# Kernel tuning notes

Measured on AMD Instinct MI355X. Metric: run time of the kernel, lower is better.

Reference implementation:

```python
import jax, jax.numpy as jnp
import numpy as np

N = 50000      # nodes
E = 400000     # directed edges
F_IN = 128     # input features
H0, C0 = 4, 64     # layer0: 4 heads x 64, concat -> 256
H1, C1 = 1, 256    # layer1: 1 head x 256, mean/concat -> 256
NCLS = 10
SLOPE = 0.2    # PyG GATConv leaky_relu negative_slope


def setup_inputs() -> dict:
    key = jax.random.key(0)
    ks = jax.random.split(key, 20)
    g = lambda k, shape, fan_in: jax.random.normal(k, shape, jnp.float32) * (1.0 / np.sqrt(fan_in))
    x = jax.random.normal(ks[0], (N, F_IN), jnp.float32)
    edge_index = jax.random.randint(ks[1], (2, E), 0, N)
    return {
        "x": x,
        "edge_index": edge_index,
        # GATConv layer 0: 128 -> 4 heads x 64, concat
        "W0": g(ks[2], (F_IN, H0 * C0), F_IN),
        "a_src0": g(ks[3], (H0, C0), C0),
        "a_dst0": g(ks[4], (H0, C0), C0),
        "b0": jnp.zeros((H0 * C0,), jnp.float32),
        # GATConv layer 1: 256 -> 1 head x 256, averaged
        "W1": g(ks[5], (H0 * C0, H1 * C1), H0 * C0),
        "a_src1": g(ks[6], (H1, C1), C1),
        "a_dst1": g(ks[7], (H1, C1), C1),
        "b1": jnp.zeros((C1,), jnp.float32),
        # MLP head 256 -> 512 -> 1024 -> NCLS
        "lw1": g(ks[8], (256, 512), 256), "lb1": jnp.zeros((512,), jnp.float32),
        "lw2": g(ks[9], (512, 1024), 512), "lb2": jnp.zeros((1024,), jnp.float32),
        "lw3": g(ks[10], (1024, NCLS), 1024), "lb3": jnp.zeros((NCLS,), jnp.float32),
    }


def _gat_conv(x, src, dst, valid, W, a_src, a_dst, b, heads, ch, concat):
    """PyG GATConv (eval mode, dropout=0): gather -> edge attention ->
    softmax over incoming edges per target -> scatter-sum aggregate."""
    n = x.shape[0]
    h = (x @ W).reshape(n, heads, ch)                      # [N,H,C]
    alpha_src = jnp.sum(h * a_src[None], axis=-1)          # [N,H]
    alpha_dst = jnp.sum(h * a_dst[None], axis=-1)          # [N,H]
    e = jax.nn.leaky_relu(alpha_src[src] + alpha_dst[dst], SLOPE)  # [Etot,H]
    e = jnp.where(valid[:, None], e, -1e9)                 # removed self-loops
    emax = jax.lax.stop_gradient(jax.ops.segment_max(e, dst, num_segments=n))
    w = jnp.exp(e - emax[dst]) * valid[:, None].astype(e.dtype)
    denom = jax.ops.segment_sum(w, dst, num_segments=n)    # [N,H] (>0: self-loops)
    w = w / denom[dst]
    out = jax.ops.segment_sum(h[src] * w[..., None], dst, num_segments=n)  # [N,H,C]
    out = out.reshape(n, heads * ch) if concat else out.mean(axis=1)
    return out + b


def reference(x, edge_index, W0, a_src0, a_dst0, b0, W1, a_src1, a_dst1, b1,
              lw1, lb1, lw2, lb2, lw3, lb3):
    n = x.shape[0]
    s0, d0 = edge_index[0], edge_index[1]
    loop = jnp.arange(n, dtype=s0.dtype)
    src = jnp.concatenate([s0, loop])
    dst = jnp.concatenate([d0, loop])
    valid = jnp.concatenate([s0 != d0, jnp.ones((n,), bool)])  # remove+add self-loops
    h = jax.nn.relu(_gat_conv(x, src, dst, valid, W0, a_src0, a_dst0, b0, H0, C0, True))
    h = jax.nn.relu(_gat_conv(h, src, dst, valid, W1, a_src1, a_dst1, b1, H1, C1, False))
    h = jax.nn.relu(h @ lw1 + lb1)
    h = jax.nn.relu(h @ lw2 + lb2)
    h = jax.nn.relu(h @ lw3 + lb3)
    return jax.nn.softmax(h, axis=1)
```

## Files before the change

kernel.cpp:

```cpp
#include <hip/hip_runtime.h>
#include <cstdint>
#include <cstddef>

#define F_IN   128
#define SLOPE  0.2f

typedef unsigned short u16;
typedef __attribute__((ext_vector_type(8))) short     bf16x8;
typedef __attribute__((ext_vector_type(8))) unsigned short u16x8;
typedef __attribute__((ext_vector_type(4))) unsigned short u16x4;
typedef __attribute__((ext_vector_type(4))) float     f32x4;

__device__ __forceinline__ u16 f2bf(float f) {
    unsigned u = __float_as_uint(f);
    unsigned r = u + 0x7FFFu + ((u >> 16) & 1u);
    return (u16)(r >> 16);
}
__device__ __forceinline__ float bf2f(u16 h) {
    return __uint_as_float(((unsigned)h) << 16);
}

__device__ __forceinline__ float lrelu(float v) { return v >= 0.f ? v : SLOPE * v; }

__global__ void alphas0_k(const u16* __restrict__ h0, const float* __restrict__ a_src,
                          const float* __restrict__ a_dst, float* __restrict__ asrc,
                          float* __restrict__ adst, int N) {
    int gid = blockIdx.x * blockDim.x + threadIdx.x;
    int n = gid >> 6, lane = gid & 63;
    if (n >= N) return;
    int h = lane >> 4, c0 = lane << 2;
    u16x4 hv = *(const u16x4*)(h0 + (size_t)n * 256 + c0);
    float4 ws = *(const float4*)(a_src + c0);
    float4 wd = *(const float4*)(a_dst + c0);
    float s1 = bf2f(hv[0]) * ws.x + bf2f(hv[1]) * ws.y + bf2f(hv[2]) * ws.z + bf2f(hv[3]) * ws.w;
    float s2 = bf2f(hv[0]) * wd.x + bf2f(hv[1]) * wd.y + bf2f(hv[2]) * wd.z + bf2f(hv[3]) * wd.w;
    #pragma unroll
    for (int off = 8; off; off >>= 1) {
        s1 += __shfl_xor(s1, off);
        s2 += __shfl_xor(s2, off);
    }
    if ((lane & 15) == 0) { asrc[n * 4 + h] = s1; adst[n * 4 + h] = s2; }
}

__global__ void alphas1_k(const u16* __restrict__ h1, const float* __restrict__ a_src,
                          const float* __restrict__ a_dst, float* __restrict__ asrc,
                          float* __restrict__ adst, int N) {
    int gid = blockIdx.x * blockDim.x + threadIdx.x;
    int n = gid >> 6, lane = gid & 63;
    if (n >= N) return;
    int c0 = lane << 2;
    u16x4 hv = *(const u16x4*)(h1 + (size_t)n * 256 + c0);
    float4 ws = *(const float4*)(a_src + c0);
    float4 wd = *(const float4*)(a_dst + c0);
    float s1 = bf2f(hv[0]) * ws.x + bf2f(hv[1]) * ws.y + bf2f(hv[2]) * ws.z + bf2f(hv[3]) * ws.w;
    float s2 = bf2f(hv[0]) * wd.x + bf2f(hv[1]) * wd.y + bf2f(hv[2]) * wd.z + bf2f(hv[3]) * wd.w;
    #pragma unroll
    for (int off = 32; off; off >>= 1) {
        s1 += __shfl_xor(s1, off);
        s2 += __shfl_xor(s2, off);
    }
    if (lane == 0) { asrc[n] = s1; adst[n] = s2; }
}

__global__ void deg_init(int* __restrict__ deg, int N) {
    int i = blockIdx.x * blockDim.x + threadIdx.x;
    if (i < N) deg[i] = 1;
}

__global__ void count_deg(const int* __restrict__ ei, int* __restrict__ deg, int E) {
    int e = blockIdx.x * blockDim.x + threadIdx.x;
    if (e >= E) return;
    int s = ei[e], d = ei[E + e];
    if (s != d) atomicAdd(&deg[d], 1);
}

__global__ void scan1(const int* __restrict__ deg, int* __restrict__ part,
                      int* __restrict__ bsum, int N) {
    __shared__ int sm[256];
    int i = blockIdx.x * 256 + threadIdx.x;
    int v = (i < N) ? deg[i] : 0;
    sm[threadIdx.x] = v; __syncthreads();
    for (int off = 1; off < 256; off <<= 1) {
        int tv = (threadIdx.x >= off) ? sm[threadIdx.x - off] : 0;
        __syncthreads();
        sm[threadIdx.x] += tv;
        __syncthreads();
    }
    if (i < N) part[i] = sm[threadIdx.x] - v;
    if (threadIdx.x == 255) bsum[blockIdx.x] = sm[255];
}

__global__ void scan2(int* __restrict__ bsum, int nb) {
    __shared__ int sm[256];
    __shared__ int carry;
    if (threadIdx.x == 0) carry = 0;
    __syncthreads();
    for (int base = 0; base < nb; base += 256) {
        int i = base + threadIdx.x;
        int v = (i < nb) ? bsum[i] : 0;
        sm[threadIdx.x] = v; __syncthreads();
        for (int off = 1; off < 256; off <<= 1) {
            int tv = (threadIdx.x >= off) ? sm[threadIdx.x - off] : 0;
            __syncthreads();
            sm[threadIdx.x] += tv;
            __syncthreads();
        }
        if (i < nb) bsum[i] = sm[threadIdx.x] - v + carry;
        __syncthreads();
        if (threadIdx.x == 0) carry += sm[255];
        __syncthreads();
    }
}

__global__ void scan3(const int* __restrict__ deg, const int* __restrict__ part,
                      const int* __restrict__ bsum, int* __restrict__ rowp,
                      int* __restrict__ cursor, int N) {
    int i = blockIdx.x * blockDim.x + threadIdx.x;
    if (i >= N) return;
    int r = part[i] + bsum[i >> 8];
    rowp[i] = r;
    cursor[i] = r;
    if (i == N - 1) rowp[N] = r + deg[i];
}

__global__ void scatter_k(const int* __restrict__ ei, int* __restrict__ cursor,
                          int* __restrict__ csr, int E, int N) {
    int e = blockIdx.x * blockDim.x + threadIdx.x;
    if (e >= E + N) return;
    int s, d;
    if (e < E) { s = ei[e]; d = ei[E + e]; if (s == d) return; }
    else       { s = d = e - E; }
    int pos = atomicAdd(&cursor[d], 1);
    csr[pos] = s;
}

__global__ void gat_gather0(const int* __restrict__ csr, const int* __restrict__ rowp,
                            const u16* __restrict__ h0, const float* __restrict__ asrc,
                            const float* __restrict__ adst, const float* __restrict__ b,
                            float* __restrict__ outx, int N) {
    int gid = blockIdx.x * blockDim.x + threadIdx.x;
    int n = gid >> 6, lane = gid & 63;
    if (n >= N) return;
    int h = lane >> 4, c0 = lane << 2;
    int beg = rowp[n], end = rowp[n + 1];
    float4 ad = *(const float4*)(adst + (size_t)n * 4);
    float m0 = -1e30f, m1 = -1e30f, m2 = -1e30f, m3 = -1e30f;
    for (int i = beg + lane; i < end; i += 64) {
        int s = csr[i];
        float4 as = *(const float4*)(asrc + (size_t)s * 4);
        m0 = fmaxf(m0, lrelu(as.x + ad.x));
        m1 = fmaxf(m1, lrelu(as.y + ad.y));
        m2 = fmaxf(m2, lrelu(as.z + ad.z));
        m3 = fmaxf(m3, lrelu(as.w + ad.w));
    }
    #pragma unroll
    for (int off = 32; off; off >>= 1) {
        m0 = fmaxf(m0, __shfl_xor(m0, off));
        m1 = fmaxf(m1, __shfl_xor(m1, off));
        m2 = fmaxf(m2, __shfl_xor(m2, off));
        m3 = fmaxf(m3, __shfl_xor(m3, off));
    }
    float mh  = (h == 0) ? m0   : (h == 1) ? m1   : (h == 2) ? m2   : m3;
    float adh = (h == 0) ? ad.x : (h == 1) ? ad.y : (h == 2) ? ad.z : ad.w;
    float acc0 = 0.f, acc1 = 0.f, acc2 = 0.f, acc3 = 0.f, den = 0.f;
    #pragma unroll 2
    for (int i = beg; i < end; ++i) {
        int s = csr[i];
        float w = __expf(lrelu(asrc[(size_t)s * 4 + h] + adh) - mh);
        den += w;
        u16x4 hv = *(const u16x4*)(h0 + (size_t)s * 256 + c0);
        acc0 += w * bf2f(hv[0]);
        acc1 += w * bf2f(hv[1]);
        acc2 += w * bf2f(hv[2]);
        acc3 += w * bf2f(hv[3]);
    }
    float inv = 1.f / den;
    float4 bb = *(const float4*)(b + c0);
    float4 ov;
    ov.x = acc0 * inv + bb.x; ov.x = ov.x > 0.f ? ov.x : 0.f;
    ov.y = acc1 * inv + bb.y; ov.y = ov.y > 0.f ? ov.y : 0.f;
    ov.z = acc2 * inv + bb.z; ov.z = ov.z > 0.f ? ov.z : 0.f;
    ov.w = acc3 * inv + bb.w; ov.w = ov.w > 0.f ? ov.w : 0.f;
    *(float4*)(outx + (size_t)n * 256 + c0) = ov;
}

__global__ void gat_gather1(const int* __restrict__ csr, const int* __restrict__ rowp,
                            const u16* __restrict__ h1, const float* __restrict__ asrc,
                            const float* __restrict__ adst, const float* __restrict__ b,
                            u16* __restrict__ outx, int N) {
    int gid = blockIdx.x * blockDim.x + threadIdx.x;
    int n = gid >> 6, lane = gid & 63;
    if (n >= N) return;
    int c0 = lane << 2;
    int beg = rowp[n], end = rowp[n + 1];
    float adn = adst[n];
    float mx = -1e30f;
    for (int i = beg + lane; i < end; i += 64) {
        int s = csr[i];
        mx = fmaxf(mx, lrelu(asrc[s] + adn));
    }
    #pragma unroll
    for (int off = 32; off; off >>= 1) mx = fmaxf(mx, __shfl_xor(mx, off));
    float acc0 = 0.f, acc1 = 0.f, acc2 = 0.f, acc3 = 0.f, den = 0.f;
    #pragma unroll 2
    for (int i = beg; i < end; ++i) {
        int s = csr[i];
        float w = __expf(lrelu(asrc[s] + adn) - mx);
        den += w;
        u16x4 hv = *(const u16x4*)(h1 + (size_t)s * 256 + c0);
        acc0 += w * bf2f(hv[0]);
        acc1 += w * bf2f(hv[1]);
        acc2 += w * bf2f(hv[2]);
        acc3 += w * bf2f(hv[3]);
    }
    float inv = 1.f / den;
    float4 bb = *(const float4*)(b + c0);
    float v0 = acc0 * inv + bb.x, v1 = acc1 * inv + bb.y;
    float v2 = acc2 * inv + bb.z, v3 = acc3 * inv + bb.w;
    u16x4 ov;
    ov[0] = f2bf(v0 > 0.f ? v0 : 0.f);
    ov[1] = f2bf(v1 > 0.f ? v1 : 0.f);
    ov[2] = f2bf(v2 > 0.f ? v2 : 0.f);
    ov[3] = f2bf(v3 > 0.f ? v3 : 0.f);
    *(u16x4*)(outx + (size_t)n * 256 + c0) = ov;
}

__global__ void pack_w(const float* __restrict__ W, u16* __restrict__ out,
                       int K, int Nsrc, int NT) {
    int gid  = blockIdx.x * blockDim.x + threadIdx.x;
    int lane = gid & 63, frag = gid >> 6;
    int KT = K >> 5;
    if (frag >= KT * NT) return;
    int nt = frag % NT, kt = frag / NT;
    int n  = nt * 16 + (lane & 15);
    int k0 = kt * 32 + ((lane >> 4) << 3);
    u16x8 v8;
    #pragma unroll
    for (int i = 0; i < 8; ++i) {
        float v = (n < Nsrc) ? W[(size_t)(k0 + i) * Nsrc + n] : 0.f;
        v8[i] = f2bf(v);
    }
    *(u16x8*)(out + (size_t)(frag * 64 + lane) * 8) = v8;
}

__global__ void pack_w_hl(const float* __restrict__ W, u16* __restrict__ ohi,
                          u16* __restrict__ olo, int K, int Nsrc, int NT) {
    int gid  = blockIdx.x * blockDim.x + threadIdx.x;
    int lane = gid & 63, frag = gid >> 6;
    int KT = K >> 5;
    if (frag >= KT * NT) return;
    int nt = frag % NT, kt = frag / NT;
    int n  = nt * 16 + (lane & 15);
    int k0 = kt * 32 + ((lane >> 4) << 3);
    u16x8 h8, l8;
    #pragma unroll
    for (int i = 0; i < 8; ++i) {
        float v = (n < Nsrc) ? W[(size_t)(k0 + i) * Nsrc + n] : 0.f;
        u16 hi = f2bf(v);
        h8[i] = hi;
        l8[i] = f2bf(v - bf2f(hi));
    }
    *(u16x8*)(ohi + (size_t)(frag * 64 + lane) * 8) = h8;
    *(u16x8*)(olo + (size_t)(frag * 64 + lane) * 8) = l8;
}

__device__ __forceinline__ bf16x8 lds_afrag(const u16* buf, int Kdim, int row0, int kt, int lane) {
    int row = row0 + (lane & 15);
    int k   = kt * 32 + ((lane >> 4) << 3);
    int idx = (row * Kdim + k) ^ ((row & 7) << 3);
    return *(const bf16x8*)(buf + idx);
}

__global__ __launch_bounds__(512) void gemm_mfma(
    const float* __restrict__ A, const u16* __restrict__ bhi, const u16* __restrict__ blo,
    u16* __restrict__ C, int M, int K) {
    __shared__ __align__(16) u16 Ahi[64 * 256];
    __shared__ __align__(16) u16 Alo[64 * 256];
    int t = threadIdx.x, lane = t & 63, w = t >> 6;
    int row0 = blockIdx.x * 64;
    int K4 = K >> 2;

    for (int idx = t; idx < 64 * K4; idx += 512) {
        int row = idx / K4, kq = (idx % K4) << 2;
        int gr = row0 + row;
        float4 v = make_float4(0.f, 0.f, 0.f, 0.f);
        if (gr < M) v = *(const float4*)(A + (size_t)gr * K + kq);
        u16x4 h4, l4;
        float vv[4] = {v.x, v.y, v.z, v.w};
        #pragma unroll
        for (int i = 0; i < 4; ++i) {
            u16 hi = f2bf(vv[i]);
            h4[i] = hi;
            l4[i] = f2bf(vv[i] - bf2f(hi));
        }
        int sidx = (row * K + kq) ^ ((row & 7) << 3);
        *(u16x4*)(Ahi + sidx) = h4;
        *(u16x4*)(Alo + sidx) = l4;
    }
    __syncthreads();

    int KT = K >> 5;
    f32x4 acc[4][2] = {};
    for (int kt = 0; kt < KT; ++kt) {
        bf16x8 ah[4], al[4];
        #pragma unroll
        for (int mt = 0; mt < 4; ++mt) {
            ah[mt] = lds_afrag(Ahi, K, mt * 16, kt, lane);
            al[mt] = lds_afrag(Alo, K, mt * 16, kt, lane);
        }
        #pragma unroll
        for (int nt = 0; nt < 2; ++nt) {
            int ntg = w * 2 + nt;
            size_t fo = ((size_t)(kt * 16 + ntg) * 64 + lane) * 8;
            bf16x8 bh = *(const bf16x8*)(bhi + fo);
            bf16x8 bl = *(const bf16x8*)(blo + fo);
            #pragma unroll
            for (int mt = 0; mt < 4; ++mt) {
                acc[mt][nt] = __builtin_amdgcn_mfma_f32_16x16x32_bf16(al[mt], bh, acc[mt][nt], 0, 0, 0);
                acc[mt][nt] = __builtin_amdgcn_mfma_f32_16x16x32_bf16(ah[mt], bl, acc[mt][nt], 0, 0, 0);
                acc[mt][nt] = __builtin_amdgcn_mfma_f32_16x16x32_bf16(ah[mt], bh, acc[mt][nt], 0, 0, 0);
            }
        }
    }

    #pragma unroll
    for (int mt = 0; mt < 4; ++mt)
        #pragma unroll
        for (int nt = 0; nt < 2; ++nt) {
            int col = w * 32 + nt * 16 + (lane & 15);
            #pragma unroll
            for (int j = 0; j < 4; ++j) {
                int gr = row0 + mt * 16 + ((lane >> 4) << 2) + j;
                if (gr < M) C[(size_t)gr * 256 + col] = f2bf(acc[mt][nt][j]);
            }
        }
}

#define NB 32

__global__ __launch_bounds__(512) void mlp_mfma(
    const u16* __restrict__ m0,
    const u16* __restrict__ w1p, const float* __restrict__ lb1,
    const u16* __restrict__ w2p, const float* __restrict__ lb2,
    const u16* __restrict__ w3p, const float* __restrict__ lb3,
    float* __restrict__ out, int N) {
    __shared__ __align__(16) u16 ldsA0[32 * 256];
    __shared__ __align__(16) u16 ldsA1[32 * 512];
    __shared__ __align__(16) u16 ldsA2[32 * 1024];
    __shared__ float slog[32 * 16];

    int t = threadIdx.x, lane = t & 63, w = t >> 6;
    int nb = blockIdx.x * NB;

    slog[t] = 0.f;

    bf16x8 b1A[4], b1B[4];
    #pragma unroll
    for (int nt = 0; nt < 4; ++nt)
        b1A[nt] = *(const bf16x8*)(w1p + ((size_t)(w * 4 + nt) * 64 + lane) * 8);

    #pragma unroll
    for (int u = 0; u < 2; ++u) {
        int unit = t + u * 512;
        int row = unit >> 5, kb = (unit & 31) << 3;
        int gn = nb + row;
        u16x8 v8;
        if (gn < N) v8 = *(const u16x8*)(m0 + (size_t)gn * 256 + kb);
        else        v8 = (u16x8)0;
        int idx = (row * 256 + kb) ^ ((row & 7) << 3);
        *(u16x8*)(ldsA0 + idx) = v8;
    }
    __syncthreads();

    f32x4 acc1[2][4] = {};
    for (int kt = 0; kt < 8; kt += 2) {
        #pragma unroll
        for (int nt = 0; nt < 4; ++nt)
            b1B[nt] = *(const bf16x8*)(w1p + ((size_t)((kt + 1) * 32 + w * 4 + nt) * 64 + lane) * 8);
        {
            bf16x8 a0 = lds_afrag(ldsA0, 256, 0,  kt, lane);
            bf16x8 a1 = lds_afrag(ldsA0, 256, 16, kt, lane);
            #pragma unroll
            for (int nt = 0; nt < 4; ++nt) {
                acc1[0][nt] = __builtin_amdgcn_mfma_f32_16x16x32_bf16(a0, b1A[nt], acc1[0][nt], 0, 0, 0);
                acc1[1][nt] = __builtin_amdgcn_mfma_f32_16x16x32_bf16(a1, b1A[nt], acc1[1][nt], 0, 0, 0);
            }
        }
        if (kt + 2 < 8) {
            #pragma unroll
            for (int nt = 0; nt < 4; ++nt)
                b1A[nt] = *(const bf16x8*)(w1p + ((size_t)((kt + 2) * 32 + w * 4 + nt) * 64 + lane) * 8);
        }
        {
            bf16x8 a0 = lds_afrag(ldsA0, 256, 0,  kt + 1, lane);
            bf16x8 a1 = lds_afrag(ldsA0, 256, 16, kt + 1, lane);
            #pragma unroll
            for (int nt = 0; nt < 4; ++nt) {
                acc1[0][nt] = __builtin_amdgcn_mfma_f32_16x16x32_bf16(a0, b1B[nt], acc1[0][nt], 0, 0, 0);
                acc1[1][nt] = __builtin_amdgcn_mfma_f32_16x16x32_bf16(a1, b1B[nt], acc1[1][nt], 0, 0, 0);
            }
        }
    }

    bf16x8 b2A[8], b2B[8];
    #pragma unroll
    for (int nt = 0; nt < 8; ++nt)
        b2A[nt] = *(const bf16x8*)(w2p + ((size_t)(w * 8 + nt) * 64 + lane) * 8);

    #pragma unroll
    for (int mt = 0; mt < 2; ++mt)
        #pragma unroll
        for (int nt = 0; nt < 4; ++nt) {
            int col = w * 64 + nt * 16 + (lane & 15);
            float bv = lb1[col];
            #pragma unroll
            for (int j = 0; j < 4; ++j) {
                int row = mt * 16 + ((lane >> 4) << 2) + j;
                float v = acc1[mt][nt][j] + bv;
                v = v > 0.f ? v : 0.f;
                ldsA1[(row * 512 + col) ^ ((row & 7) << 3)] = f2bf(v);
            }
        }
    __syncthreads();

    f32x4 acc2[2][8] = {};
    for (int kt = 0; kt < 16; kt += 2) {
        #pragma unroll
        for (int nt = 0; nt < 8; ++nt)
            b2B[nt] = *(const bf16x8*)(w2p + ((size_t)((kt + 1) * 64 + w * 8 + nt) * 64 + lane) * 8);
        {
            bf16x8 a0 = lds_afrag(ldsA1, 512, 0,  kt, lane);
            bf16x8 a1 = lds_afrag(ldsA1, 512, 16, kt, lane);
            #pragma unroll
            for (int nt = 0; nt < 8; ++nt) {
                acc2[0][nt] = __builtin_amdgcn_mfma_f32_16x16x32_bf16(a0, b2A[nt], acc2[0][nt], 0, 0, 0);
                acc2[1][nt] = __builtin_amdgcn_mfma_f32_16x16x32_bf16(a1, b2A[nt], acc2[1][nt], 0, 0, 0);
            }
        }
        if (kt + 2 < 16) {
            #pragma unroll
            for (int nt = 0; nt < 8; ++nt)
                b2A[nt] = *(const bf16x8*)(w2p + ((size_t)((kt + 2) * 64 + w * 8 + nt) * 64 + lane) * 8);
        }
        {
            bf16x8 a0 = lds_afrag(ldsA1, 512, 0,  kt + 1, lane);
            bf16x8 a1 = lds_afrag(ldsA1, 512, 16, kt + 1, lane);
            #pragma unroll
            for (int nt = 0; nt < 8; ++nt) {
                acc2[0][nt] = __builtin_amdgcn_mfma_f32_16x16x32_bf16(a0, b2B[nt], acc2[0][nt], 0, 0, 0);
                acc2[1][nt] = __builtin_amdgcn_mfma_f32_16x16x32_bf16(a1, b2B[nt], acc2[1][nt], 0, 0, 0);
            }
        }
    }

    bf16x8 b3[4];
    #pragma unroll
    for (int kk = 0; kk < 4; ++kk)
        b3[kk] = *(const bf16x8*)(w3p + ((size_t)(w * 4 + kk) * 64 + lane) * 8);

    #pragma unroll
    for (int mt = 0; mt < 2; ++mt)
        #pragma unroll
        for (int nt = 0; nt < 8; ++nt) {
            int col = w * 128 + nt * 16 + (lane & 15);
            float bv = lb2[col];
            #pragma unroll
            for (int j = 0; j < 4; ++j) {
                int row = mt * 16 + ((lane >> 4) << 2) + j;
                float v = acc2[mt][nt][j] + bv;
                v = v > 0.f ? v : 0.f;
                ldsA2[(row * 1024 + col) ^ ((row & 7) << 3)] = f2bf(v);
            }
        }
    __syncthreads();

    {
        f32x4 acc[2] = {};
        #pragma unroll
        for (int kk = 0; kk < 4; ++kk) {
            int kt = w * 4 + kk;
            bf16x8 a0 = lds_afrag(ldsA2, 1024, 0,  kt, lane);
            bf16x8 a1 = lds_afrag(ldsA2, 1024, 16, kt, lane);
            acc[0] = __builtin_amdgcn_mfma_f32_16x16x32_bf16(a0, b3[kk], acc[0], 0, 0, 0);
            acc[1] = __builtin_amdgcn_mfma_f32_16x16x32_bf16(a1, b3[kk], acc[1], 0, 0, 0);
        }
        int col = lane & 15;
        #pragma unroll
        for (int mt = 0; mt < 2; ++mt)
            #pragma unroll
            for (int j = 0; j < 4; ++j) {
                int row = mt * 16 + ((lane >> 4) << 2) + j;
                atomicAdd(&slog[row * 16 + col], acc[mt][j]);
            }
    }
    __syncthreads();

    if (t < 32) {
        int gn = nb + t;
        if (gn < N) {
            float lg[10], m = -1e30f;
            #pragma unroll
            for (int k = 0; k < 10; ++k) {
                float v = slog[t * 16 + k] + lb3[k];
                v = v > 0.f ? v : 0.f;
                lg[k] = v;
                if (v > m) m = v;
            }
            float ssum = 0.f;
            #pragma unroll
            for (int k = 0; k < 10; ++k) { lg[k] = __expf(lg[k] - m); ssum += lg[k]; }
            float inv = 1.f / ssum;
            #pragma unroll
            for (int k = 0; k < 10; ++k) out[(size_t)gn * 10 + k] = lg[k] * inv;
        }
    }
}

extern "C" void kernel_launch(void* const* d_in, const int* in_sizes, int n_in,
                              void* d_out, int out_size, void* d_ws, size_t ws_size,
                              hipStream_t stream) {
    const float* x       = (const float*)d_in[0];
    const int*   ei      = (const int*)  d_in[1];
    const float* W0      = (const float*)d_in[2];
    const float* a_src0  = (const float*)d_in[3];
    const float* a_dst0  = (const float*)d_in[4];
    const float* b0      = (const float*)d_in[5];
    const float* W1      = (const float*)d_in[6];
    const float* a_src1  = (const float*)d_in[7];
    const float* a_dst1  = (const float*)d_in[8];
    const float* b1      = (const float*)d_in[9];
    const float* lw1     = (const float*)d_in[10];
    const float* lb1     = (const float*)d_in[11];
    const float* lw2     = (const float*)d_in[12];
    const float* lb2     = (const float*)d_in[13];
    const float* lw3     = (const float*)d_in[14];
    const float* lb3     = (const float*)d_in[15];
    float*       out     = (float*)d_out;

    const int N  = in_sizes[0] / F_IN;
    const int E  = in_sizes[1] / 2;
    const int ET = E + N;

    char* base = (char*)d_ws;
    size_t szHb = (size_t)N * 256 * sizeof(u16);
    u16*   hbf  = (u16*)base;
    float* bufG = (float*)(base + szHb);
    u16*   m0b  = (u16*)(base + szHb + (size_t)N * 256 * sizeof(float));
    float* asrc = (float*)(base + 2 * szHb + (size_t)N * 256 * sizeof(float));
    float* adst = asrc + (size_t)N * 4;
    u16*   w1p  = (u16*)(adst + (size_t)N * 4);
    u16*   w2p  = w1p + 256 * 512;
    u16*   w3p  = w2p + 512 * 1024;
    u16*   w0h  = w3p + 1024 * 16;
    u16*   w0l  = w0h + 128 * 256;
    u16*   w1h  = w0l + 128 * 256;
    u16*   w1l  = w1h + 256 * 256;
    int*   deg  = (int*)(w1l + 256 * 256);
    int*   rowp   = deg + N;
    int*   cursor = rowp + N + 1;
    int*   part   = cursor + N;
    int*   bsum   = part + N;
    int*   csr    = bsum + 256;

    const int TB  = 256;
    const int nb1 = (N + 255) / 256;
    const int gemm_grid = (N + 63) / 64;

    pack_w<<<(8  * 32 * 64 + TB - 1) / TB, TB, 0, stream>>>(lw1, w1p, 256,  512,  32);
    pack_w<<<(16 * 64 * 64 + TB - 1) / TB, TB, 0, stream>>>(lw2, w2p, 512,  1024, 64);
    pack_w<<<(32 * 1  * 64 + TB - 1) / TB, TB, 0, stream>>>(lw3, w3p, 1024, 10,   1);
    pack_w_hl<<<(4 * 16 * 64 + TB - 1) / TB, TB, 0, stream>>>(W0, w0h, w0l, 128, 256, 16);
    pack_w_hl<<<(8 * 16 * 64 + TB - 1) / TB, TB, 0, stream>>>(W1, w1h, w1l, 256, 256, 16);

    deg_init<<<nb1, TB, 0, stream>>>(deg, N);
    count_deg<<<(E + TB - 1) / TB, TB, 0, stream>>>(ei, deg, E);
    scan1<<<nb1, TB, 0, stream>>>(deg, part, bsum, N);
    scan2<<<1, TB, 0, stream>>>(bsum, nb1);
    scan3<<<nb1, TB, 0, stream>>>(deg, part, bsum, rowp, cursor, N);
    scatter_k<<<(ET + TB - 1) / TB, TB, 0, stream>>>(ei, cursor, csr, E, N);

    gemm_mfma<<<gemm_grid, 512, 0, stream>>>(x, w0h, w0l, hbf, N, 128);
    alphas0_k<<<(N * 64 + TB - 1) / TB, TB, 0, stream>>>(hbf, a_src0, a_dst0, asrc, adst, N);
    gat_gather0<<<((size_t)N * 64 + TB - 1) / TB, TB, 0, stream>>>(csr, rowp, hbf, asrc, adst, b0, bufG, N);

    gemm_mfma<<<gemm_grid, 512, 0, stream>>>(bufG, w1h, w1l, hbf, N, 256);
    alphas1_k<<<(N * 64 + TB - 1) / TB, TB, 0, stream>>>(hbf, a_src1, a_dst1, asrc, adst, N);
    gat_gather1<<<((size_t)N * 64 + TB - 1) / TB, TB, 0, stream>>>(csr, rowp, hbf, asrc, adst, b1, m0b, N);

    mlp_mfma<<<(N + NB - 1) / NB, 512, 0, stream>>>(m0b, w1p, lb1, w2p, lb2, w3p, lb3, out, N);
}
```

Before: 372.8 us.

## Split fused MLP into 64-row MFMA layers 1-2 kernel and separate layer-3 softmax kernel

Replaces the fully fused 32-row MLP kernel with a 64-row kernel computing layers 1 and 2 (writing the 1024-wide activation to global memory in bf16) plus a per-node wavefront kernel for the final 10-class layer and softmax. Work is processed in two halves so the intermediate fits in the reused workspace buffer. The larger row tile raises weight reuse per MFMA and removes LDS atomics, at the cost of extra global round-trip traffic for the intermediate and loss of the previous weight-load double buffering.

```diff
diff --git a/kernel.cpp b/kernel.cpp
--- a/kernel.cpp
+++ b/kernel.cpp
@@ -336,183 +336,136 @@
         }
 }
 
-#define NB 32
-
-__global__ __launch_bounds__(512) void mlp_mfma(
+__global__ __launch_bounds__(512) void mlp12(
     const u16* __restrict__ m0,
     const u16* __restrict__ w1p, const float* __restrict__ lb1,
     const u16* __restrict__ w2p, const float* __restrict__ lb2,
-    const u16* __restrict__ w3p, const float* __restrict__ lb3,
-    float* __restrict__ out, int N) {
-    __shared__ __align__(16) u16 ldsA0[32 * 256];
-    __shared__ __align__(16) u16 ldsA1[32 * 512];
-    __shared__ __align__(16) u16 ldsA2[32 * 1024];
-    __shared__ float slog[32 * 16];
+    u16* __restrict__ h2, int nbase, int M) {
+    __shared__ __align__(16) u16 ldsIn[64 * 256];
+    __shared__ __align__(16) u16 ldsA1[64 * 512];
 
     int t = threadIdx.x, lane = t & 63, w = t >> 6;
-    int nb = blockIdx.x * NB;
-
-    slog[t] = 0.f;
-
-    bf16x8 b1A[4], b1B[4];
-    #pragma unroll
-    for (int nt = 0; nt < 4; ++nt)
-        b1A[nt] = *(const bf16x8*)(w1p + ((size_t)(w * 4 + nt) * 64 + lane) * 8);
-
-    #pragma unroll
-    for (int u = 0; u < 2; ++u) {
+    int rb = blockIdx.x * 64;
+
+    #pragma unroll
+    for (int u = 0; u < 4; ++u) {
         int unit = t + u * 512;
         int row = unit >> 5, kb = (unit & 31) << 3;
-        int gn = nb + row;
+        int r = rb + row;
         u16x8 v8;
-        if (gn < N) v8 = *(const u16x8*)(m0 + (size_t)gn * 256 + kb);
-        else        v8 = (u16x8)0;
+        if (r < M) v8 = *(const u16x8*)(m0 + (size_t)(nbase + r) * 256 + kb);
+        else       v8 = (u16x8)0;
         int idx = (row * 256 + kb) ^ ((row & 7) << 3);
-        *(u16x8*)(ldsA0 + idx) = v8;
+        *(u16x8*)(ldsIn + idx) = v8;
     }
     __syncthreads();
 
-    f32x4 acc1[2][4] = {};
-    for (int kt = 0; kt < 8; kt += 2) {
-        #pragma unroll
-        for (int nt = 0; nt < 4; ++nt)
-            b1B[nt] = *(const bf16x8*)(w1p + ((size_t)((kt + 1) * 32 + w * 4 + nt) * 64 + lane) * 8);
-        {
-            bf16x8 a0 = lds_afrag(ldsA0, 256, 0,  kt, lane);
-            bf16x8 a1 = lds_afrag(ldsA0, 256, 16, kt, lane);
+    {
+        f32x4 acc1[4][4] = {};
+        for (int kt = 0; kt < 8; ++kt) {
+            bf16x8 a[4];
+            #pragma unroll
+            for (int mt = 0; mt < 4; ++mt) a[mt] = lds_afrag(ldsIn, 256, mt * 16, kt, lane);
             #pragma unroll
             for (int nt = 0; nt < 4; ++nt) {
-                acc1[0][nt] = __builtin_amdgcn_mfma_f32_16x16x32_bf16(a0, b1A[nt], acc1[0][nt], 0, 0, 0);
-                acc1[1][nt] = __builtin_amdgcn_mfma_f32_16x16x32_bf16(a1, b1A[nt], acc1[1][nt], 0, 0, 0);
+                bf16x8 b = *(const bf16x8*)(w1p + ((size_t)(kt * 32 + w * 4 + nt) * 64 + lane) * 8);
+                #pragma unroll
+                for (int mt = 0; mt < 4; ++mt)
+                    acc1[mt][nt] = __builtin_amdgcn_mfma_f32_16x16x32_bf16(a[mt], b, acc1[mt][nt], 0, 0, 0);
             }
         }
-        if (kt + 2 < 8) {
-            #pragma unroll
-            for (int nt = 0; nt < 4; ++nt)
-                b1A[nt] = *(const bf16x8*)(w1p + ((size_t)((kt + 2) * 32 + w * 4 + nt) * 64 + lane) * 8);
-        }
-        {
-            bf16x8 a0 = lds_afrag(ldsA0, 256, 0,  kt + 1, lane);
-            bf16x8 a1 = lds_afrag(ldsA0, 256, 16, kt + 1, lane);
+        #pragma unroll
+        for (int mt = 0; mt < 4; ++mt)
             #pragma unroll
             for (int nt = 0; nt < 4; ++nt) {
-                acc1[0][nt] = __builtin_amdgcn_mfma_f32_16x16x32_bf16(a0, b1B[nt], acc1[0][nt], 0, 0, 0);
-                acc1[1][nt] = __builtin_amdgcn_mfma_f32_16x16x32_bf16(a1, b1B[nt], acc1[1][nt], 0, 0, 0);
+                int col = w * 64 + nt * 16 + (lane & 15);
+                float bv = lb1[col];
+                #pragma unroll
+                for (int j = 0; j < 4; ++j) {
+                    int row = mt * 16 + ((lane >> 4) << 2) + j;
+                    float v = acc1[mt][nt][j] + bv;
+                    v = v > 0.f ? v : 0.f;
+                    ldsA1[(row * 512 + col) ^ ((row & 7) << 3)] = f2bf(v);
+                }
             }
-        }
-    }
-
-    bf16x8 b2A[8], b2B[8];
-    #pragma unroll
-    for (int nt = 0; nt < 8; ++nt)
-        b2A[nt] = *(const bf16x8*)(w2p + ((size_t)(w * 8 + nt) * 64 + lane) * 8);
-
-    #pragma unroll
-    for (int mt = 0; mt < 2; ++mt)
-        #pragma unroll
-        for (int nt = 0; nt < 4; ++nt) {
-            int col = w * 64 + nt * 16 + (lane & 15);
-            float bv = lb1[col];
-            #pragma unroll
-            for (int j = 0; j < 4; ++j) {
-                int row = mt * 16 + ((lane >> 4) << 2) + j;
-                float v = acc1[mt][nt][j] + bv;
-                v = v > 0.f ? v : 0.f;
-                ldsA1[(row * 512 + col) ^ ((row & 7) << 3)] = f2bf(v);
+    }
+    __syncthreads();
+
+    for (int ch = 0; ch < 2; ++ch) {
+        f32x4 acc[4][4] = {};
+        for (int kt = 0; kt < 16; ++kt) {
+            bf16x8 a[4];
+            #pragma unroll
+            for (int mt = 0; mt < 4; ++mt) a[mt] = lds_afrag(ldsA1, 512, mt * 16, kt, lane);
+            #pragma unroll
+            for (int nt = 0; nt < 4; ++nt) {
+                int ntg = ch * 32 + w * 4 + nt;
+                bf16x8 b = *(const bf16x8*)(w2p + ((size_t)(kt * 64 + ntg) * 64 + lane) * 8);
+                #pragma unroll
+                for (int mt = 0; mt < 4; ++mt)
+                    acc[mt][nt] = __builtin_amdgcn_mfma_f32_16x16x32_bf16(a[mt], b, acc[mt][nt], 0, 0, 0);
             }
         }
-    __syncthreads();
-
-    f32x4 acc2[2][8] = {};
-    for (int kt = 0; kt < 16; kt += 2) {
-        #pragma unroll
-        for (int nt = 0; nt < 8; ++nt)
-            b2B[nt] = *(const bf16x8*)(w2p + ((size_t)((kt + 1) * 64 + w * 8 + nt) * 64 + lane) * 8);
-        {
-            bf16x8 a0 = lds_afrag(ldsA1, 512, 0,  kt, lane);
-            bf16x8 a1 = lds_afrag(ldsA1, 512, 16, kt, lane);
-            #pragma unroll
-            for (int nt = 0; nt < 8; ++nt) {
-                acc2[0][nt] = __builtin_amdgcn_mfma_f32_16x16x32_bf16(a0, b2A[nt], acc2[0][nt], 0, 0, 0);
-                acc2[1][nt] = __builtin_amdgcn_mfma_f32_16x16x32_bf16(a1, b2A[nt], acc2[1][nt], 0, 0, 0);
+        #pragma unroll
+        for (int mt = 0; mt < 4; ++mt)
+            #pragma unroll
+            for (int nt = 0; nt < 4; ++nt) {
+                int col = ch * 512 + w * 64 + nt * 16 + (lane & 15);
+                float bv = lb2[col];
+                #pragma unroll
+                for (int j = 0; j < 4; ++j) {
+                    int r = rb + mt * 16 + ((lane >> 4) << 2) + j;
+                    if (r < M) {
+                        float v = acc[mt][nt][j] + bv;
+                        v = v > 0.f ? v : 0.f;
+                        h2[(size_t)r * 1024 + col] = f2bf(v);
+                    }
+                }
             }
-        }
-        if (kt + 2 < 16) {
-            #pragma unroll
-            for (int nt = 0; nt < 8; ++nt)
-                b2A[nt] = *(const bf16x8*)(w2p + ((size_t)((kt + 2) * 64 + w * 8 + nt) * 64 + lane) * 8);
-        }
-        {
-            bf16x8 a0 = lds_afrag(ldsA1, 512, 0,  kt + 1, lane);
-            bf16x8 a1 = lds_afrag(ldsA1, 512, 16, kt + 1, lane);
-            #pragma unroll
-            for (int nt = 0; nt < 8; ++nt) {
-                acc2[0][nt] = __builtin_amdgcn_mfma_f32_16x16x32_bf16(a0, b2B[nt], acc2[0][nt], 0, 0, 0);
-                acc2[1][nt] = __builtin_amdgcn_mfma_f32_16x16x32_bf16(a1, b2B[nt], acc2[1][nt], 0, 0, 0);
-            }
-        }
-    }
-
-    bf16x8 b3[4];
-    #pragma unroll
-    for (int kk = 0; kk < 4; ++kk)
-        b3[kk] = *(const bf16x8*)(w3p + ((size_t)(w * 4 + kk) * 64 + lane) * 8);
-
-    #pragma unroll
-    for (int mt = 0; mt < 2; ++mt)
-        #pragma unroll
-        for (int nt = 0; nt < 8; ++nt) {
-            int col = w * 128 + nt * 16 + (lane & 15);
-            float bv = lb2[col];
-            #pragma unroll
-            for (int j = 0; j < 4; ++j) {
-                int row = mt * 16 + ((lane >> 4) << 2) + j;
-                float v = acc2[mt][nt][j] + bv;
-                v = v > 0.f ? v : 0.f;
-                ldsA2[(row * 1024 + col) ^ ((row & 7) << 3)] = f2bf(v);
-            }
-        }
-    __syncthreads();
-
-    {
-        f32x4 acc[2] = {};
-        #pragma unroll
-        for (int kk = 0; kk < 4; ++kk) {
-            int kt = w * 4 + kk;
-            bf16x8 a0 = lds_afrag(ldsA2, 1024, 0,  kt, lane);
-            bf16x8 a1 = lds_afrag(ldsA2, 1024, 16, kt, lane);
-            acc[0] = __builtin_amdgcn_mfma_f32_16x16x32_bf16(a0, b3[kk], acc[0], 0, 0, 0);
-            acc[1] = __builtin_amdgcn_mfma_f32_16x16x32_bf16(a1, b3[kk], acc[1], 0, 0, 0);
-        }
-        int col = lane & 15;
-        #pragma unroll
-        for (int mt = 0; mt < 2; ++mt)
-            #pragma unroll
-            for (int j = 0; j < 4; ++j) {
-                int row = mt * 16 + ((lane >> 4) << 2) + j;
-                atomicAdd(&slog[row * 16 + col], acc[mt][j]);
-            }
-    }
-    __syncthreads();
-
-    if (t < 32) {
-        int gn = nb + t;
-        if (gn < N) {
-            float lg[10], m = -1e30f;
-            #pragma unroll
-            for (int k = 0; k < 10; ++k) {
-                float v = slog[t * 16 + k] + lb3[k];
-                v = v > 0.f ? v : 0.f;
-                lg[k] = v;
-                if (v > m) m = v;
-            }
-            float ssum = 0.f;
-            #pragma unroll
-            for (int k = 0; k < 10; ++k) { lg[k] = __expf(lg[k] - m); ssum += lg[k]; }
-            float inv = 1.f / ssum;
-            #pragma unroll
-            for (int k = 0; k < 10; ++k) out[(size_t)gn * 10 + k] = lg[k] * inv;
-        }
+    }
+}
+
+__global__ __launch_bounds__(256) void mlp3(
+    const u16* __restrict__ h2, const float* __restrict__ lw3, const float* __restrict__ lb3,
+    float* __restrict__ out, int nbase, int M) {
+    int gid = blockIdx.x * blockDim.x + threadIdx.x;
+    int n = gid >> 6, lane = gid & 63;
+    if (n >= M) return;
+    const u16* hp = h2 + (size_t)n * 1024 + lane * 16;
+    u16x8 v0 = *(const u16x8*)hp;
+    u16x8 v1 = *(const u16x8*)(hp + 8);
+    float x[16];
+    #pragma unroll
+    for (int i = 0; i < 8; ++i) { x[i] = bf2f(v0[i]); x[8 + i] = bf2f(v1[i]); }
+    float lg[10];
+    #pragma unroll
+    for (int k = 0; k < 10; ++k) lg[k] = 0.f;
+    const float* wp = lw3 + (size_t)lane * 16 * 10;
+    #pragma unroll
+    for (int i = 0; i < 16; ++i) {
+        #pragma unroll
+        for (int k = 0; k < 10; ++k) lg[k] += x[i] * wp[i * 10 + k];
+    }
+    #pragma unroll
+    for (int k = 0; k < 10; ++k) {
+        #pragma unroll
+        for (int off = 32; off; off >>= 1) lg[k] += __shfl_xor(lg[k], off);
+    }
+    if (lane == 0) {
+        float m = -1e30f;
+        #pragma unroll
+        for (int k = 0; k < 10; ++k) {
+            float v = lg[k] + lb3[k];
+            v = v > 0.f ? v : 0.f;
+            lg[k] = v;
+            if (v > m) m = v;
+        }
+        float ssum = 0.f;
+        #pragma unroll
+        for (int k = 0; k < 10; ++k) { lg[k] = __expf(lg[k] - m); ssum += lg[k]; }
+        float inv = 1.f / ssum;
+        #pragma unroll
+        for (int k = 0; k < 10; ++k) out[(size_t)(nbase + n) * 10 + k] = lg[k] * inv;
     }
 }
 
@@ -550,8 +503,7 @@
     float* adst = asrc + (size_t)N * 4;
     u16*   w1p  = (u16*)(adst + (size_t)N * 4);
     u16*   w2p  = w1p + 256 * 512;
-    u16*   w3p  = w2p + 512 * 1024;
-    u16*   w0h  = w3p + 1024 * 16;
+    u16*   w0h  = w2p + 512 * 1024;
     u16*   w0l  = w0h + 128 * 256;
     u16*   w1h  = w0l + 128 * 256;
     u16*   w1l  = w1h + 256 * 256;
@@ -561,14 +513,15 @@
     int*   part   = cursor + N;
     int*   bsum   = part + N;
     int*   csr    = bsum + 256;
+    u16*   h2     = (u16*)bufG;
 
     const int TB  = 256;
     const int nb1 = (N + 255) / 256;
     const int gemm_grid = (N + 63) / 64;
+    const int HALF = 25000;
 
     pack_w<<<(8  * 32 * 64 + TB - 1) / TB, TB, 0, stream>>>(lw1, w1p, 256,  512,  32);
     pack_w<<<(16 * 64 * 64 + TB - 1) / TB, TB, 0, stream>>>(lw2, w2p, 512,  1024, 64);
-    pack_w<<<(32 * 1  * 64 + TB - 1) / TB, TB, 0, stream>>>(lw3, w3p, 1024, 10,   1);
     pack_w_hl<<<(4 * 16 * 64 + TB - 1) / TB, TB, 0, stream>>>(W0, w0h, w0l, 128, 256, 16);
     pack_w_hl<<<(8 * 16 * 64 + TB - 1) / TB, TB, 0, stream>>>(W1, w1h, w1l, 256, 256, 16);
 
@@ -587,5 +540,10 @@
     alphas1_k<<<(N * 64 + TB - 1) / TB, TB, 0, stream>>>(hbf, a_src1, a_dst1, asrc, adst, N);
     gat_gather1<<<((size_t)N * 64 + TB - 1) / TB, TB, 0, stream>>>(csr, rowp, hbf, asrc, adst, b1, m0b, N);
 
-    mlp_mfma<<<(N + NB - 1) / NB, 512, 0, stream>>>(m0b, w1p, lb1, w2p, lb2, w3p, lb3, out, N);
-}
+    for (int half = 0; half < 2; ++half) {
+        int nbase = half * HALF;
+        int M     = (half == 0) ? HALF : (N - HALF);
+        mlp12<<<(M + 63) / 64, 512, 0, stream>>>(m0b, w1p, lb1, w2p, lb2, h2, nbase, M);
+        mlp3<<<((size_t)M * 64 + TB - 1) / TB, TB, 0, stream>>>(h2, lw3, lb3, out, nbase, M);
+    }
+}
```

New measurement: 784.0 us. 110% more time.
